# Kernel optimization log

Measured on AMD Instinct MI355X. Metric: run time of the kernel, lower is better.

The kernel has to match this reference:

```python
import jax, jax.numpy as jnp
import numpy as np

B, S, D, H, W, L, V = 4, 8192, 256, 8, 64, 6, 256
DH = D // H          # head dim 32
NW = S // W          # number of windows
FF = 4 * D


def setup_inputs() -> dict:
    key = jax.random.key(0)
    ks = jax.random.split(key, 12)
    w = lambda k, shape: (jax.random.normal(k, shape, jnp.float32) * 0.02)
    return {
        "input_ids": jax.random.randint(ks[0], (B, S), 0, V).astype(jnp.int32),
        "attention_mask": jnp.ones((B, S), jnp.int32),
        "word_start": jax.random.randint(ks[1], (B, S), 0, 2).astype(jnp.int32),
        "emb": w(ks[2], (V, D)),
        "pos_emb": w(ks[3], (S, D)),
        "ln1_g": jnp.ones((L, D)), "ln1_b": jnp.zeros((L, D)),
        "wq": w(ks[4], (L, D, D)), "wk": w(ks[5], (L, D, D)),
        "wv": w(ks[6], (L, D, D)), "wo": w(ks[7], (L, D, D)),
        "ln2_g": jnp.ones((L, D)), "ln2_b": jnp.zeros((L, D)),
        "w1": w(ks[8], (L, D, FF)), "b1": jnp.zeros((L, FF)),
        "w2": w(ks[9], (L, FF, D)), "b2": jnp.zeros((L, D)),
        "lnf_g": jnp.ones((D,)), "lnf_b": jnp.zeros((D,)),
    }


def _ln(x, g, b):
    m = jnp.mean(x, -1, keepdims=True)
    v = jnp.mean((x - m) ** 2, -1, keepdims=True)
    return (x - m) * jax.lax.rsqrt(v + 1e-5) * g + b


def _local_attn(x, mask_bool, wq, wk, wv, wo):
    # non-causal local attention: each 64-token window attends to
    # [prev window, own window, next window] (look_backward=1, look_forward=1)
    def heads(t):
        return t.reshape(B, S, H, DH).transpose(0, 2, 1, 3)  # [B,H,S,DH]
    q = heads(x @ wq)
    k = heads(x @ wk)
    v = heads(x @ wv)
    qw = q.reshape(B, H, NW, W, DH)

    def ctx(t):  # gather 3-window key/value context
        tw = t.reshape(B, H, NW, W, DH)
        tp = jnp.pad(tw, ((0, 0), (0, 0), (1, 1), (0, 0), (0, 0)))
        return jnp.concatenate([tp[:, :, i:i + NW] for i in range(3)], axis=3)  # [B,H,NW,3W,DH]

    kc, vc = ctx(k), ctx(v)
    mw = mask_bool.reshape(B, NW, W)
    mp = jnp.pad(mw, ((0, 0), (1, 1), (0, 0)))
    mc = jnp.concatenate([mp[:, i:i + NW] for i in range(3)], axis=2)  # [B,NW,3W]

    scores = jnp.einsum('bhnwd,bhnkd->bhnwk', qw, kc) * (DH ** -0.5)
    scores = jnp.where(mc[:, None, :, None, :], scores, -1e9)
    attn = jax.nn.softmax(scores, axis=-1)
    o = jnp.einsum('bhnwk,bhnkd->bhnwd', attn, vc)
    o = o.reshape(B, H, S, DH).transpose(0, 2, 1, 3).reshape(B, S, D)
    return o @ wo


def _gather_word_starts(x, ws):
    # pack hidden states at word-start positions to the front, zero-padded
    def one(xb, wb):
        idx = jnp.cumsum(wb) - 1
        tgt = jnp.where(wb > 0, idx, S)  # invalid rows go to scratch slot S
        return jnp.zeros((S + 1, xb.shape[-1]), xb.dtype).at[tgt].set(xb)[:S]
    return jax.vmap(one)(x, ws)


def reference(input_ids, attention_mask, word_start, emb, pos_emb,
              ln1_g, ln1_b, wq, wk, wv, wo, ln2_g, ln2_b,
              w1, b1, w2, b2, lnf_g, lnf_b):
    mask_bool = attention_mask > 0
    x = emb[input_ids] + pos_emb[None, :, :]
    for i in range(L):
        x = x + _local_attn(_ln(x, ln1_g[i], ln1_b[i]), mask_bool,
                            wq[i], wk[i], wv[i], wo[i])
        h = _ln(x, ln2_g[i], ln2_b[i])
        x = x + jax.nn.gelu(h @ w1[i] + b1[i]) @ w2[i] + b2[i]
    x = _ln(x, lnf_g, lnf_b)
    return _gather_word_starts(x, word_start)
```

## Files before the change

kernel.cpp:

```cpp
#include <hip/hip_runtime.h>


#define S_LEN 8192
#define BATCH 4
#define DMODEL 256
#define NHEAD 8
#define WIN 64
#define NWIN 128
#define NLAYER 6
#define FFDIM 1024
#define MROWS (BATCH * S_LEN)

typedef float __attribute__((ext_vector_type(4))) f32x4;
typedef unsigned int __attribute__((ext_vector_type(2))) u32x2;
typedef unsigned short u16;
typedef unsigned short __attribute__((ext_vector_type(4))) u16x4;

__device__ __forceinline__ u16 f2bf(float f) {
  unsigned u = __builtin_bit_cast(unsigned, f);
  u += 0x7fffu + ((u >> 16) & 1u);
  return (u16)(u >> 16);
}

__device__ __forceinline__ unsigned cvt_pk_bf16(float lo, float hi) {
  unsigned r;
  asm("v_cvt_pk_bf16_f32 %0, %1, %2" : "=v"(r) : "v"(lo), "v"(hi));
  return r;
}
__device__ __forceinline__ u32x2 pack_bf16x4(f32x4 v) {
  u32x2 o;
  o[0] = cvt_pk_bf16(v[0], v[1]);
  o[1] = cvt_pk_bf16(v[2], v[3]);
  return o;
}
__device__ __forceinline__ f32x4 unpack_bf16x4(u16x4 h) {
  f32x4 o;
  o[0] = __builtin_bit_cast(float, (unsigned)h[0] << 16);
  o[1] = __builtin_bit_cast(float, (unsigned)h[1] << 16);
  o[2] = __builtin_bit_cast(float, (unsigned)h[2] << 16);
  o[3] = __builtin_bit_cast(float, (unsigned)h[3] << 16);
  return o;
}

__device__ __forceinline__ void mfma16(f32x4& d, f32x4 a, f32x4 b) {
  asm volatile("v_mfma_f32_16x16x32_bf16 %0, %1, %2, %0"
               : "+v"(d) : "v"(a), "v"(b));
}
#define MFMA_FENCE() asm volatile("s_nop 7\n\ts_nop 7")

__device__ __forceinline__ void gload_lds16(const void* g, void* l) {
  __builtin_amdgcn_global_load_lds(
      (__attribute__((address_space(1))) void*)g,
      (__attribute__((address_space(3))) void*)l, 16, 0, 0);
}

__device__ __forceinline__ float gelu_f(float t) {
  float u = 0.7978845608028654f * (t + 0.044715f * t * t * t);
  float e = __expf(-2.0f * u);
  return t * __builtin_amdgcn_rcpf(1.0f + e);
}

__global__ __launch_bounds__(256) void embed_ln_kernel(
    const int* __restrict__ ids, const float* __restrict__ emb,
    const float* __restrict__ pos, const float* __restrict__ g,
    const float* __restrict__ b, u16* __restrict__ x, u16* __restrict__ xb) {
  int wid = threadIdx.x >> 6, lane = threadIdx.x & 63;
  int r = blockIdx.x * 4 + wid;
  int s = r & (S_LEN - 1);
  int id = ids[r];
  f32x4 e = *(const f32x4*)(emb + (size_t)id * DMODEL + lane * 4);
  f32x4 p = *(const f32x4*)(pos + (size_t)s * DMODEL + lane * 4);
  f32x4 v = e + p;
  *(u32x2*)(x + (size_t)r * DMODEL + lane * 4) = pack_bf16x4(v);
  float sm = v[0] + v[1] + v[2] + v[3];
  float q = v[0] * v[0] + v[1] * v[1] + v[2] * v[2] + v[3] * v[3];
  for (int off = 32; off; off >>= 1) {
    sm += __shfl_xor(sm, off, 64);
    q += __shfl_xor(q, off, 64);
  }
  float mean = sm * (1.0f / DMODEL);
  float var = q * (1.0f / DMODEL) - mean * mean;
  float rs = rsqrtf(var + 1e-5f);
  f32x4 gg = *(const f32x4*)(g + lane * 4);
  f32x4 bb = *(const f32x4*)(b + lane * 4);
  f32x4 o;
  for (int j = 0; j < 4; ++j) o[j] = (v[j] - mean) * rs * gg[j] + bb[j];
  *(u32x2*)(xb + (size_t)r * DMODEL + lane * 4) = pack_bf16x4(o);
}

__global__ void zero_kernel(float* __restrict__ p, int n4) {
  int i = blockIdx.x * blockDim.x + threadIdx.x;
  int stride = gridDim.x * blockDim.x;
  f32x4 z = {0.f, 0.f, 0.f, 0.f};
  for (; i < n4; i += stride) ((f32x4*)p)[i] = z;
}

__global__ void tcast_kernel(const float* __restrict__ src, u16* __restrict__ dst,
                             int total, int K, int N, int dls, int rowOff) {
  int i = blockIdx.x * blockDim.x + threadIdx.x;
  int stride = gridDim.x * blockDim.x;
  int KN = K * N;
  for (; i < total; i += stride) {
    int l = i / KN;
    int rem = i - l * KN;
    int k = rem / N;
    int n = rem - k * N;
    dst[l * dls + (rowOff + n) * K + k] = f2bf(src[i]);
  }
}

template <bool GELU_ACT, bool HAS_BIAS>
__global__ __launch_bounds__(256) void gemm_bf16(
    const u16* __restrict__ A, const u16* __restrict__ Bt,
    u16* __restrict__ C, const float* __restrict__ bias,
    int N, int K, int nx) {
  __shared__ u16 As[128 * 64];
  __shared__ u16 Bs[128 * 64];

  int nwg = gridDim.x;
  int bid = blockIdx.x;
  int w8 = (bid & 7) * (nwg >> 3) + (bid >> 3);
  int cx = w8 % nx, ry = w8 / nx;
  int bm = ry * 128, bn = cx * 128;

  int tid = threadIdx.x, lane = tid & 63, wid = tid >> 6;
  int l15 = lane & 15, l4 = lane >> 4;
  int wm = wid >> 1, wn = wid & 1;

  const u16* Ab = A + (size_t)bm * K;
  const u16* Bb = Bt + (size_t)bn * K;

  f32x4 acc[4][4] = {};

  for (int kt = 0; kt < K; kt += 64) {
#pragma unroll
    for (int i = 0; i < 4; ++i) {
      int s = tid + i * 256;
      int r = s >> 3, c = (s & 7) ^ (r & 7);
      gload_lds16(Ab + (size_t)r * K + kt + c * 8,
                  (char*)As + (wid * 64 + i * 256) * 16);
    }
#pragma unroll
    for (int i = 0; i < 4; ++i) {
      int s = tid + i * 256;
      int r = s >> 3, c = (s & 7) ^ (r & 7);
      gload_lds16(Bb + (size_t)r * K + kt + c * 8,
                  (char*)Bs + (wid * 64 + i * 256) * 16);
    }
    __syncthreads();
#pragma unroll
    for (int t = 0; t < 2; ++t) {
      f32x4 af[4], bf[4];
#pragma unroll
      for (int m = 0; m < 4; ++m) {
        int r = wm * 64 + m * 16 + l15;
        af[m] = ((const f32x4*)As)[r * 8 + ((t * 4 + l4) ^ (r & 7))];
      }
#pragma unroll
      for (int n = 0; n < 4; ++n) {
        int r = wn * 64 + n * 16 + l15;
        bf[n] = ((const f32x4*)Bs)[r * 8 + ((t * 4 + l4) ^ (r & 7))];
      }
#pragma unroll
      for (int m = 0; m < 4; ++m)
#pragma unroll
        for (int n = 0; n < 4; ++n) mfma16(acc[m][n], bf[n], af[m]);
    }
    __syncthreads();
  }
  MFMA_FENCE();

  int colB = bn + wn * 64;
  f32x4 bv[4];
#pragma unroll
  for (int n = 0; n < 4; ++n)
    bv[n] = HAS_BIAS ? *(const f32x4*)(bias + colB + n * 16 + l4 * 4)
                     : (f32x4){0.f, 0.f, 0.f, 0.f};
#pragma unroll
  for (int m = 0; m < 4; ++m) {
    int row = bm + wm * 64 + m * 16 + l15;
#pragma unroll
    for (int n = 0; n < 4; ++n) {
      f32x4 v = acc[m][n] + bv[n];
      if (GELU_ACT) {
#pragma unroll
        for (int j = 0; j < 4; ++j) v[j] = gelu_f(v[j]);
      }
      *(u32x2*)(C + (size_t)row * N + colB + n * 16 + l4 * 4) = pack_bf16x4(v);
    }
  }
}

template <bool DO_LN>
__global__ __launch_bounds__(256) void gemm_res_ln(
    const u16* __restrict__ A, const u16* __restrict__ Bt,
    u16* __restrict__ x, u16* __restrict__ xb,
    const float* __restrict__ bias, const float* __restrict__ g,
    const float* __restrict__ b, int K) {
  __shared__ u16 As[64 * 64];
  __shared__ u16 Bs[256 * 64];
  __shared__ float redS[64][4];
  __shared__ float redQ[64][4];

  int nwg = gridDim.x;
  int bid = blockIdx.x;
  int bm = ((bid & 7) * (nwg >> 3) + (bid >> 3)) * 64;

  int tid = threadIdx.x, lane = tid & 63, wid = tid >> 6;
  int l15 = lane & 15, l4 = lane >> 4;

  const u16* Ab = A + (size_t)bm * K;
  f32x4 acc[4][4] = {};

  for (int kt = 0; kt < K; kt += 64) {
#pragma unroll
    for (int i = 0; i < 2; ++i) {
      int s = tid + i * 256;
      int r = s >> 3, c = (s & 7) ^ (r & 7);
      gload_lds16(Ab + (size_t)r * K + kt + c * 8,
                  (char*)As + (wid * 64 + i * 256) * 16);
    }
#pragma unroll
    for (int i = 0; i < 8; ++i) {
      int s = tid + i * 256;
      int r = s >> 3, c = (s & 7) ^ (r & 7);
      gload_lds16(Bt + (size_t)r * K + kt + c * 8,
                  (char*)Bs + (wid * 64 + i * 256) * 16);
    }
    __syncthreads();
#pragma unroll
    for (int t = 0; t < 2; ++t) {
      f32x4 af[4], bf[4];
#pragma unroll
      for (int m = 0; m < 4; ++m) {
        int r = m * 16 + l15;
        af[m] = ((const f32x4*)As)[r * 8 + ((t * 4 + l4) ^ (r & 7))];
      }
#pragma unroll
      for (int n = 0; n < 4; ++n) {
        int r = wid * 64 + n * 16 + l15;
        bf[n] = ((const f32x4*)Bs)[r * 8 + ((t * 4 + l4) ^ (r & 7))];
      }
#pragma unroll
      for (int m = 0; m < 4; ++m)
#pragma unroll
        for (int n = 0; n < 4; ++n) mfma16(acc[m][n], bf[n], af[m]);
    }
    __syncthreads();
  }
  MFMA_FENCE();

  int colB = wid * 64;
  f32x4 bv[4];
#pragma unroll
  for (int n = 0; n < 4; ++n)
    bv[n] = bias ? *(const f32x4*)(bias + colB + n * 16 + l4 * 4)
                 : (f32x4){0.f, 0.f, 0.f, 0.f};

#pragma unroll
  for (int m = 0; m < 4; ++m) {
    int r = m * 16 + l15;
    size_t rowoff = (size_t)(bm + r) * DMODEL + colB;
    float s = 0.f, q = 0.f;
#pragma unroll
    for (int n = 0; n < 4; ++n) {
      f32x4 xv = unpack_bf16x4(*(const u16x4*)(x + rowoff + n * 16 + l4 * 4));
      f32x4 v = acc[m][n] + bv[n] + xv;
      acc[m][n] = v;
      s += v[0] + v[1] + v[2] + v[3];
      q += v[0] * v[0] + v[1] * v[1] + v[2] * v[2] + v[3] * v[3];
    }
    if (DO_LN) {
      s += __shfl_xor(s, 16, 64);
      s += __shfl_xor(s, 32, 64);
      q += __shfl_xor(q, 16, 64);
      q += __shfl_xor(q, 32, 64);
      if (l4 == 0) {
        redS[r][wid] = s;
        redQ[r][wid] = q;
      }
    }
  }
  if (DO_LN) __syncthreads();

  f32x4 gv[4], bbv[4];
  if (DO_LN) {
#pragma unroll
    for (int n = 0; n < 4; ++n) {
      gv[n] = *(const f32x4*)(g + colB + n * 16 + l4 * 4);
      bbv[n] = *(const f32x4*)(b + colB + n * 16 + l4 * 4);
    }
  }
#pragma unroll
  for (int m = 0; m < 4; ++m) {
    int r = m * 16 + l15;
    size_t rowoff = (size_t)(bm + r) * DMODEL + colB;
    float mean = 0.f, rs = 0.f;
    if (DO_LN) {
      f32x4 sv = *(const f32x4*)redS[r];
      f32x4 qv = *(const f32x4*)redQ[r];
      float ssum = sv[0] + sv[1] + sv[2] + sv[3];
      float qsum = qv[0] + qv[1] + qv[2] + qv[3];
      mean = ssum * (1.0f / DMODEL);
      float var = qsum * (1.0f / DMODEL) - mean * mean;
      rs = rsqrtf(var + 1e-5f);
    }
#pragma unroll
    for (int n = 0; n < 4; ++n) {
      f32x4 v = acc[m][n];
      *(u32x2*)(x + rowoff + n * 16 + l4 * 4) = pack_bf16x4(v);
      if (DO_LN) {
        f32x4 o;
#pragma unroll
        for (int j = 0; j < 4; ++j)
          o[j] = (v[j] - mean) * rs * gv[n][j] + bbv[n][j];
        *(u32x2*)(xb + rowoff + n * 16 + l4 * 4) = pack_bf16x4(o);
      }
    }
  }
}

__global__ __launch_bounds__(256, 4) void attn_kernel(
    const u16* __restrict__ qkv, const int* __restrict__ amask,
    u16* __restrict__ ao) {
  int win = blockIdx.x, h = blockIdx.y, b = blockIdx.z;
  int tid = threadIdx.x, lane = tid & 63, wid = tid >> 6;
  int l15 = lane & 15, l4 = lane >> 4;

  __shared__ u16 KPs[64 * 216];
  __shared__ u16 Vts[32 * 200];
  __shared__ unsigned char valid[192];

  int t0 = win * WIN - WIN;

  if (tid < 192) {
    int t = t0 + tid;
    valid[tid] = (t >= 0 && t < S_LEN && amask[b * S_LEN + t] != 0) ? 1 : 0;
  }
#pragma unroll
  for (int cc = 0; cc < 3; ++cc) {
    int chunk = cc * 256 + tid;
    int key = chunk >> 2, c = chunk & 3;
    int t = t0 + key;
    t = t < 0 ? 0 : (t >= S_LEN ? S_LEN - 1 : t);
    f32x4 kd = *(const f32x4*)(qkv + (size_t)(b * S_LEN + t) * 768 + 256 + h * 32 + c * 8);
    *(f32x4*)(KPs + key * 40 + c * 8) = kd;
  }
  for (int e = tid; e < 192 * 32; e += 256) {
    int key = e >> 5, d = e & 31;
    int t = t0 + key;
    t = t < 0 ? 0 : (t >= S_LEN ? S_LEN - 1 : t);
    Vts[d * 200 + key] = qkv[(size_t)(b * S_LEN + t) * 768 + 512 + h * 32 + d];
  }
  __syncthreads();

  int qrow = b * S_LEN + win * WIN + wid * 16 + l15;
  f32x4 aq = *(const f32x4*)(qkv + (size_t)qrow * 768 + h * 32 + l4 * 8);

  f32x4 sacc[12] = {};
#pragma unroll
  for (int f = 0; f < 12; ++f) {
    f32x4 bk = *(const f32x4*)(KPs + (f * 16 + l15) * 40 + l4 * 8);
    mfma16(sacc[f], bk, aq);
  }
  MFMA_FENCE();

  const float scale = 0.17677669529663687f;
  float mrow = -1e30f;
#pragma unroll
  for (int f = 0; f < 12; ++f) {
    const unsigned char* vp = &valid[f * 16 + l4 * 4];
#pragma unroll
    for (int j = 0; j < 4; ++j) {
      float sv = vp[j] ? sacc[f][j] * scale : -1e9f;
      sacc[f][j] = sv;
      mrow = fmaxf(mrow, sv);
    }
  }
  mrow = fmaxf(mrow, __shfl_xor(mrow, 16, 64));
  mrow = fmaxf(mrow, __shfl_xor(mrow, 32, 64));

  float ssum = 0.f;
#pragma unroll
  for (int f = 0; f < 12; ++f)
#pragma unroll
    for (int j = 0; j < 4; ++j) {
      float p = __expf(sacc[f][j] - mrow);
      sacc[f][j] = p;
      ssum += p;
    }
  ssum += __shfl_xor(ssum, 16, 64);
  ssum += __shfl_xor(ssum, 32, 64);

  __syncthreads();

#pragma unroll
  for (int f = 0; f < 12; ++f) {
    u32x2 pk;
    pk[0] = cvt_pk_bf16(sacc[f][0], sacc[f][1]);
    pk[1] = cvt_pk_bf16(sacc[f][2], sacc[f][3]);
    *(u32x2*)(KPs + (wid * 16 + l15) * 216 + f * 16 + l4 * 4) = pk;
  }
  __syncthreads();

  f32x4 oacc[2] = {};
#pragma unroll
  for (int kk = 0; kk < 6; ++kk) {
    f32x4 ap = *(const f32x4*)(KPs + (wid * 16 + l15) * 216 + kk * 32 + l4 * 8);
#pragma unroll
    for (int nf = 0; nf < 2; ++nf) {
      f32x4 bvv = *(const f32x4*)(Vts + (nf * 16 + l15) * 200 + kk * 32 + l4 * 8);
      mfma16(oacc[nf], bvv, ap);
    }
  }
  MFMA_FENCE();

  float invv = 1.0f / ssum;
  size_t obase = (size_t)qrow * 256 + h * 32;
#pragma unroll
  for (int nf = 0; nf < 2; ++nf) {
    f32x4 v = oacc[nf] * invv;
    *(u32x2*)(ao + obase + nf * 16 + l4 * 4) = pack_bf16x4(v);
  }
}

__global__ __launch_bounds__(256) void scan_kernel(const int* __restrict__ wsrt,
                                                   int* __restrict__ tgt) {
  __shared__ int part[256];
  int b = blockIdx.x, tid = threadIdx.x;
  const int* src = wsrt + b * S_LEN;
  int* dst = tgt + b * S_LEN;
  int base = tid * 32;
  int loc[32];
  int s = 0;
#pragma unroll
  for (int i = 0; i < 32; ++i) {
    loc[i] = src[base + i];
    s += loc[i];
  }
  part[tid] = s;
  __syncthreads();
  for (int off = 1; off < 256; off <<= 1) {
    int v = (tid >= off) ? part[tid - off] : 0;
    __syncthreads();
    part[tid] += v;
    __syncthreads();
  }
  int cum = part[tid] - s;
#pragma unroll
  for (int i = 0; i < 32; ++i) {
    cum += loc[i];
    dst[base + i] = (loc[i] > 0) ? (cum - 1) : -1;
  }
}

__global__ __launch_bounds__(64) void gather_ln_kernel(
    const u16* __restrict__ x, const int* __restrict__ tgt,
    const float* __restrict__ g, const float* __restrict__ b,
    float* __restrict__ out) {
  int r = blockIdx.x;
  int tg = tgt[r];
  if (tg < 0) return;
  int bIdx = r >> 13;
  int lane = threadIdx.x;
  f32x4 v = unpack_bf16x4(*(const u16x4*)(x + (size_t)r * DMODEL + lane * 4));
  float s = v[0] + v[1] + v[2] + v[3];
  float q = v[0] * v[0] + v[1] * v[1] + v[2] * v[2] + v[3] * v[3];
  for (int off = 32; off; off >>= 1) {
    s += __shfl_xor(s, off, 64);
    q += __shfl_xor(q, off, 64);
  }
  float mean = s * (1.0f / DMODEL);
  float var = q * (1.0f / DMODEL) - mean * mean;
  float rs = rsqrtf(var + 1e-5f);
  f32x4 gg = *(const f32x4*)(g + lane * 4);
  f32x4 bb = *(const f32x4*)(b + lane * 4);
  f32x4 o;
  for (int j = 0; j < 4; ++j) o[j] = (v[j] - mean) * rs * gg[j] + bb[j];
  *(f32x4*)(out + (size_t)(bIdx * S_LEN + tg) * DMODEL + lane * 4) = o;
}

extern "C" void kernel_launch(void* const* d_in, const int* in_sizes, int n_in,
                              void* d_out, int out_size, void* d_ws,
                              size_t ws_size, hipStream_t stream) {
  const int* ids = (const int*)d_in[0];
  const int* amask = (const int*)d_in[1];
  const int* wstart = (const int*)d_in[2];
  const float* emb = (const float*)d_in[3];
  const float* pos = (const float*)d_in[4];
  const float* ln1g = (const float*)d_in[5];
  const float* ln1b = (const float*)d_in[6];
  const float* wq = (const float*)d_in[7];
  const float* wk = (const float*)d_in[8];
  const float* wv = (const float*)d_in[9];
  const float* wo = (const float*)d_in[10];
  const float* ln2g = (const float*)d_in[11];
  const float* ln2b = (const float*)d_in[12];
  const float* w1 = (const float*)d_in[13];
  const float* b1 = (const float*)d_in[14];
  const float* w2 = (const float*)d_in[15];
  const float* b2 = (const float*)d_in[16];
  const float* lnfg = (const float*)d_in[17];
  const float* lnfb = (const float*)d_in[18];

  char* ws = (char*)d_ws;
  const size_t OFF_X = 0;
  const size_t OFF_XB = 33554432;
  const size_t OFF_AO = 50331648;
  const size_t OFF_BIG = 67108864;
  const size_t OFF_WQKVT = 134217728;
  const size_t OFF_WOT = 136577024;
  const size_t OFF_W1T = 137363456;
  const size_t OFF_W2T = 140509184;
  const size_t OFF_TGT = 143654912;
  const size_t NEEDED = 143785984;
  if (ws_size < NEEDED) return;

  u16* x = (u16*)(ws + OFF_X);
  u16* xb = (u16*)(ws + OFF_XB);
  u16* ao = (u16*)(ws + OFF_AO);
  u16* big = (u16*)(ws + OFF_BIG);
  u16* WqkvT = (u16*)(ws + OFF_WQKVT);
  u16* WoT = (u16*)(ws + OFF_WOT);
  u16* W1T = (u16*)(ws + OFF_W1T);
  u16* W2T = (u16*)(ws + OFF_W2T);
  int* tgt = (int*)(ws + OFF_TGT);

  tcast_kernel<<<1024, 256, 0, stream>>>(wq, WqkvT, NLAYER * 256 * 256, 256, 256, 768 * 256, 0);
  tcast_kernel<<<1024, 256, 0, stream>>>(wk, WqkvT, NLAYER * 256 * 256, 256, 256, 768 * 256, 256);
  tcast_kernel<<<1024, 256, 0, stream>>>(wv, WqkvT, NLAYER * 256 * 256, 256, 256, 768 * 256, 512);
  tcast_kernel<<<1024, 256, 0, stream>>>(wo, WoT, NLAYER * 256 * 256, 256, 256, 256 * 256, 0);
  tcast_kernel<<<2048, 256, 0, stream>>>(w1, W1T, NLAYER * 256 * 1024, 256, 1024, 1024 * 256, 0);
  tcast_kernel<<<2048, 256, 0, stream>>>(w2, W2T, NLAYER * 1024 * 256, 1024, 256, 256 * 1024, 0);

  embed_ln_kernel<<<MROWS / 4, 256, 0, stream>>>(ids, emb, pos, ln1g, ln1b, x, xb);
  zero_kernel<<<2048, 256, 0, stream>>>((float*)d_out, out_size / 4);
  scan_kernel<<<BATCH, 256, 0, stream>>>(wstart, tgt);

  for (int l = 0; l < NLAYER; ++l) {
    gemm_bf16<false, false><<<1536, 256, 0, stream>>>(
        xb, WqkvT + (size_t)l * 768 * 256, big, nullptr, 768, 256, 6);
    attn_kernel<<<dim3(NWIN, NHEAD, BATCH), 256, 0, stream>>>(big, amask, ao);
    gemm_res_ln<true><<<MROWS / 64, 256, 0, stream>>>(
        ao, WoT + (size_t)l * 256 * 256, x, xb, nullptr,
        ln2g + l * DMODEL, ln2b + l * DMODEL, 256);
    gemm_bf16<true, true><<<2048, 256, 0, stream>>>(
        xb, W1T + (size_t)l * 1024 * 256, big, b1 + l * FFDIM, 1024, 256, 8);
    if (l < NLAYER - 1) {
      gemm_res_ln<true><<<MROWS / 64, 256, 0, stream>>>(
          big, W2T + (size_t)l * 256 * 1024, x, xb, b2 + l * DMODEL,
          ln1g + (l + 1) * DMODEL, ln1b + (l + 1) * DMODEL, 1024);
    } else {
      gemm_res_ln<false><<<MROWS / 64, 256, 0, stream>>>(
          big, W2T + (size_t)l * 256 * 1024, x, nullptr, b2 + l * DMODEL,
          nullptr, nullptr, 1024);
    }
  }

  gather_ln_kernel<<<MROWS, 64, 0, stream>>>(x, tgt, lnfg, lnfb, (float*)d_out);
}
```

Before: 910.4 us.

## Write V transposed from QKV GEMM and swizzle attention LDS tiles

The QKV GEMM epilogue now writes the V columns straight into a transposed [B, D, S] buffer, so the attention kernel loads V with 16-byte vector reads instead of scalar strided gathers. K, P and V tiles in LDS switch to an XOR-swizzled 64-element-row layout to reduce bank conflicts. Softmax folds log2(e) into the scale, applies the mask as an additive bias with fma, and uses the native exp2 instruction. The V-transpose epilogue uses scattered 2-byte global stores with a stride of S, which may cost more in the GEMM than it saves in attention.

Result: faster. 856.9 us (-5.9%).

```diff
diff --git a/kernel.cpp b/kernel.cpp
--- a/kernel.cpp
+++ b/kernel.cpp
@@ -40,6 +40,12 @@
   o[2] = __builtin_bit_cast(float, (unsigned)h[2] << 16);
   o[3] = __builtin_bit_cast(float, (unsigned)h[3] << 16);
   return o;
+}
+
+__device__ __forceinline__ float exp2_f(float x) {
+  float r;
+  asm("v_exp_f32 %0, %1" : "=v"(r) : "v"(x));
+  return r;
 }
 
 __device__ __forceinline__ void mfma16(f32x4& d, f32x4 a, f32x4 b) {
@@ -109,10 +115,10 @@
   }
 }
 
-template <bool GELU_ACT, bool HAS_BIAS>
+template <bool GELU_ACT, bool HAS_BIAS, bool QKV>
 __global__ __launch_bounds__(256) void gemm_bf16(
     const u16* __restrict__ A, const u16* __restrict__ Bt,
-    u16* __restrict__ C, const float* __restrict__ bias,
+    u16* __restrict__ C, u16* __restrict__ Vt, const float* __restrict__ bias,
     int N, int K, int nx) {
   __shared__ u16 As[128 * 64];
   __shared__ u16 Bs[128 * 64];
@@ -171,6 +177,22 @@
   MFMA_FENCE();
 
   int colB = bn + wn * 64;
+  if (QKV && colB >= 512) {
+#pragma unroll
+    for (int m = 0; m < 4; ++m) {
+      int row = bm + wm * 64 + m * 16 + l15;
+      int bb = row >> 13, s = row & (S_LEN - 1);
+#pragma unroll
+      for (int n = 0; n < 4; ++n)
+#pragma unroll
+        for (int j = 0; j < 4; ++j) {
+          int col = colB + n * 16 + l4 * 4 + j;
+          Vt[((size_t)(bb * 256 + (col - 512))) * S_LEN + s] =
+              f2bf(acc[m][n][j]);
+        }
+    }
+    return;
+  }
   f32x4 bv[4];
 #pragma unroll
   for (int n = 0; n < 4; ++n)
@@ -321,36 +343,45 @@
 }
 
 __global__ __launch_bounds__(256, 4) void attn_kernel(
-    const u16* __restrict__ qkv, const int* __restrict__ amask,
-    u16* __restrict__ ao) {
+    const u16* __restrict__ qkv, const u16* __restrict__ vt,
+    const int* __restrict__ amask, u16* __restrict__ ao) {
   int win = blockIdx.x, h = blockIdx.y, b = blockIdx.z;
   int tid = threadIdx.x, lane = tid & 63, wid = tid >> 6;
   int l15 = lane & 15, l4 = lane >> 4;
 
-  __shared__ u16 KPs[64 * 216];
-  __shared__ u16 Vts[32 * 200];
-  __shared__ unsigned char valid[192];
+  __shared__ u16 KPs[192 * 64];
+  __shared__ u16 Vts[96 * 64];
+  __shared__ float bias[192];
 
   int t0 = win * WIN - WIN;
 
   if (tid < 192) {
     int t = t0 + tid;
-    valid[tid] = (t >= 0 && t < S_LEN && amask[b * S_LEN + t] != 0) ? 1 : 0;
-  }
-#pragma unroll
-  for (int cc = 0; cc < 3; ++cc) {
-    int chunk = cc * 256 + tid;
-    int key = chunk >> 2, c = chunk & 3;
-    int t = t0 + key;
+    bias[tid] =
+        (t >= 0 && t < S_LEN && amask[b * S_LEN + t] != 0) ? 0.0f : -1e9f;
+  }
+#pragma unroll
+  for (int it = 0; it < 3; ++it) {
+    int c = it * 256 + tid;
+    int k = c >> 2, j = c & 3;
+    int t = t0 + k;
     t = t < 0 ? 0 : (t >= S_LEN ? S_LEN - 1 : t);
-    f32x4 kd = *(const f32x4*)(qkv + (size_t)(b * S_LEN + t) * 768 + 256 + h * 32 + c * 8);
-    *(f32x4*)(KPs + key * 40 + c * 8) = kd;
-  }
-  for (int e = tid; e < 192 * 32; e += 256) {
-    int key = e >> 5, d = e & 31;
-    int t = t0 + key;
-    t = t < 0 ? 0 : (t >= S_LEN ? S_LEN - 1 : t);
-    Vts[d * 200 + key] = qkv[(size_t)(b * S_LEN + t) * 768 + 512 + h * 32 + d];
+    f32x4 kd = *(const f32x4*)(qkv + (size_t)(b * S_LEN + t) * 768 + 256 +
+                               h * 32 + j * 8);
+    int row = k >> 1;
+    int cc = (((k & 1) << 2) | j) ^ (row & 7);
+    *(f32x4*)(KPs + row * 64 + cc * 8) = kd;
+  }
+#pragma unroll
+  for (int it = 0; it < 3; ++it) {
+    int c = it * 256 + tid;
+    int d = c / 24, kc = c - d * 24;
+    int ts = t0 + kc * 8;
+    ts = ts < 0 ? 0 : (ts > S_LEN - 8 ? S_LEN - 8 : ts);
+    f32x4 vd = *(const f32x4*)(vt + ((size_t)((b * 8 + h) * 32 + d)) * S_LEN + ts);
+    int row = d * 3 + (kc >> 3);
+    int cc = (kc & 7) ^ (row & 7);
+    *(f32x4*)(Vts + row * 64 + cc * 8) = vd;
   }
   __syncthreads();
 
@@ -358,21 +389,23 @@
   f32x4 aq = *(const f32x4*)(qkv + (size_t)qrow * 768 + h * 32 + l4 * 8);
 
   f32x4 sacc[12] = {};
+  int krb = l15 >> 1;
+  int kcc = (((l15 & 1) << 2) | l4) ^ (krb & 7);
 #pragma unroll
   for (int f = 0; f < 12; ++f) {
-    f32x4 bk = *(const f32x4*)(KPs + (f * 16 + l15) * 40 + l4 * 8);
+    f32x4 bk = *(const f32x4*)(KPs + (f * 8 + krb) * 64 + kcc * 8);
     mfma16(sacc[f], bk, aq);
   }
   MFMA_FENCE();
 
-  const float scale = 0.17677669529663687f;
+  const float scale2 = 0.17677669529663687f * 1.4426950408889634f;
   float mrow = -1e30f;
 #pragma unroll
   for (int f = 0; f < 12; ++f) {
-    const unsigned char* vp = &valid[f * 16 + l4 * 4];
+    f32x4 bi = *(const f32x4*)&bias[f * 16 + l4 * 4];
 #pragma unroll
     for (int j = 0; j < 4; ++j) {
-      float sv = vp[j] ? sacc[f][j] * scale : -1e9f;
+      float sv = fmaf(sacc[f][j], scale2, bi[j]);
       sacc[f][j] = sv;
       mrow = fmaxf(mrow, sv);
     }
@@ -385,7 +418,7 @@
   for (int f = 0; f < 12; ++f)
 #pragma unroll
     for (int j = 0; j < 4; ++j) {
-      float p = __expf(sacc[f][j] - mrow);
+      float p = exp2_f(sacc[f][j] - mrow);
       sacc[f][j] = p;
       ssum += p;
     }
@@ -394,22 +427,32 @@
 
   __syncthreads();
 
+  int q = wid * 16 + l15;
 #pragma unroll
   for (int f = 0; f < 12; ++f) {
     u32x2 pk;
     pk[0] = cvt_pk_bf16(sacc[f][0], sacc[f][1]);
     pk[1] = cvt_pk_bf16(sacc[f][2], sacc[f][3]);
-    *(u32x2*)(KPs + (wid * 16 + l15) * 216 + f * 16 + l4 * 4) = pk;
+    int kc = f * 2 + (l4 >> 1);
+    int row = q * 3 + (kc >> 3);
+    int cc = (kc & 7) ^ (row & 7);
+    *(u32x2*)(KPs + row * 64 + cc * 8 + (l4 & 1) * 4) = pk;
   }
   __syncthreads();
 
   f32x4 oacc[2] = {};
 #pragma unroll
   for (int kk = 0; kk < 6; ++kk) {
-    f32x4 ap = *(const f32x4*)(KPs + (wid * 16 + l15) * 216 + kk * 32 + l4 * 8);
+    int kc = kk * 4 + l4;
+    int rowp = q * 3 + (kc >> 3);
+    int ccp = (kc & 7) ^ (rowp & 7);
+    f32x4 ap = *(const f32x4*)(KPs + rowp * 64 + ccp * 8);
 #pragma unroll
     for (int nf = 0; nf < 2; ++nf) {
-      f32x4 bvv = *(const f32x4*)(Vts + (nf * 16 + l15) * 200 + kk * 32 + l4 * 8);
+      int d = nf * 16 + l15;
+      int rowv = d * 3 + (kc >> 3);
+      int ccv = (kc & 7) ^ (rowv & 7);
+      f32x4 bvv = *(const f32x4*)(Vts + rowv * 64 + ccv * 8);
       mfma16(oacc[nf], bvv, ap);
     }
   }
@@ -508,6 +551,7 @@
   const size_t OFF_XB = 33554432;
   const size_t OFF_AO = 50331648;
   const size_t OFF_BIG = 67108864;
+  const size_t OFF_VT = 117440512;
   const size_t OFF_WQKVT = 134217728;
   const size_t OFF_WOT = 136577024;
   const size_t OFF_W1T = 137363456;
@@ -520,6 +564,7 @@
   u16* xb = (u16*)(ws + OFF_XB);
   u16* ao = (u16*)(ws + OFF_AO);
   u16* big = (u16*)(ws + OFF_BIG);
+  u16* vt = (u16*)(ws + OFF_VT);
   u16* WqkvT = (u16*)(ws + OFF_WQKVT);
   u16* WoT = (u16*)(ws + OFF_WOT);
   u16* W1T = (u16*)(ws + OFF_W1T);
@@ -538,14 +583,14 @@
   scan_kernel<<<BATCH, 256, 0, stream>>>(wstart, tgt);
 
   for (int l = 0; l < NLAYER; ++l) {
-    gemm_bf16<false, false><<<1536, 256, 0, stream>>>(
-        xb, WqkvT + (size_t)l * 768 * 256, big, nullptr, 768, 256, 6);
-    attn_kernel<<<dim3(NWIN, NHEAD, BATCH), 256, 0, stream>>>(big, amask, ao);
+    gemm_bf16<false, false, true><<<1536, 256, 0, stream>>>(
+        xb, WqkvT + (size_t)l * 768 * 256, big, vt, nullptr, 768, 256, 6);
+    attn_kernel<<<dim3(NWIN, NHEAD, BATCH), 256, 0, stream>>>(big, vt, amask, ao);
     gemm_res_ln<true><<<MROWS / 64, 256, 0, stream>>>(
         ao, WoT + (size_t)l * 256 * 256, x, xb, nullptr,
         ln2g + l * DMODEL, ln2b + l * DMODEL, 256);
-    gemm_bf16<true, true><<<2048, 256, 0, stream>>>(
-        xb, W1T + (size_t)l * 1024 * 256, big, b1 + l * FFDIM, 1024, 256, 8);
+    gemm_bf16<true, true, false><<<2048, 256, 0, stream>>>(
+        xb, W1T + (size_t)l * 1024 * 256, big, nullptr, b1 + l * FFDIM, 1024, 256, 8);
     if (l < NLAYER - 1) {
       gemm_res_ln<true><<<MROWS / 64, 256, 0, stream>>>(
           big, W2T + (size_t)l * 256 * 1024, x, xb, b2 + l * DMODEL,
```
